# Kernel optimization log

Hardware: AMD Instinct MI355X
Metric: run time of the kernel (lower is better)

The kernel has to match this reference:

```python
import jax, jax.numpy as jnp
import numpy as np

# ---- constants mirroring the module config ----
TIMESTEPS = 1000
N_GT = 3            # GT phases {stable, pre-shock, shock}
NUM_EXPERTS = 6     # 2 sub-experts per GT phase; phase L -> experts {L, L+3}
LAMBDA_REG = 0.01
LAMBDA_LB = 0.01
PHASE_WEIGHTS = np.array([1.0, 5.0, 5.0], dtype=np.float32)


def _sinusoidal_embed(t, dim):
    # standard DDPM sinusoidal timestep embedding -> [B, dim]
    half = dim // 2
    freqs = jnp.exp(-jnp.log(10000.0) * jnp.arange(half, dtype=jnp.float32) / half)
    args = t.astype(jnp.float32)[:, None] * freqs[None, :]
    return jnp.concatenate([jnp.sin(args), jnp.cos(args)], axis=-1)


def _alphas_bar():
    betas = jnp.linspace(1e-4, 0.02, TIMESTEPS, dtype=jnp.float32)
    return jnp.cumprod(1.0 - betas)


def setup_inputs() -> dict:
    B, Tp, Tf, Df, Ds, dm, E, H = 512, 256, 64, 64, 32, 512, NUM_EXPERTS, 512
    key = jax.random.key(0)
    ks = jax.random.split(key, 16)
    s = 0.02  # init scale
    d_in = Df + 2 * dm  # noisy features + global ctx + t embedding
    return {
        'observed_data': jax.random.normal(ks[0], (B, Tp, Df), jnp.float32),
        'future_data':   jax.random.normal(ks[1], (B, Tf, Df), jnp.float32),
        'static_context': jax.random.normal(ks[2], (B, Ds), jnp.float32),
        'eps':           jax.random.normal(ks[3], (B, Tf, Df), jnp.float32),
        'phase_label':   jax.random.randint(ks[4], (B,), 0, N_GT),
        't':             jax.random.randint(ks[5], (B,), 0, TIMESTEPS),
        'W_enc':    jax.random.normal(ks[6], (Df, dm), jnp.float32) * s,
        'b_enc':    jnp.zeros((dm,), jnp.float32),
        'W_stat':   jax.random.normal(ks[7], (Ds, dm), jnp.float32) * s,
        'W_router': jax.random.normal(ks[8], (dm, E), jnp.float32) * s,
        'b_router': jnp.zeros((E,), jnp.float32),
        'W1': jax.random.normal(ks[9],  (E, d_in, H), jnp.float32) * s,
        'b1': jnp.zeros((E, H), jnp.float32),
        'W2': jax.random.normal(ks[10], (E, H, Df), jnp.float32) * s,
        'b2': jnp.zeros((E, Df), jnp.float32),
    }


def reference(observed_data, future_data, static_context, eps,
              W_enc, b_enc, W_stat, W_router, b_router,
              W1, b1, W2, b2, phase_label, t):
    B, Tf, Df = future_data.shape
    E = W1.shape[0]
    dm = W_enc.shape[1]

    # ---- frozen encoder (torch.no_grad in the original) ----
    ctx_seq = jax.nn.gelu(observed_data @ W_enc + (static_context @ W_stat)[:, None, :] + b_enc)  # [B,Tp,dm]
    global_ctx = ctx_seq.mean(axis=1)                                                             # [B,dm]
    ctx_seq = jax.lax.stop_gradient(ctx_seq)
    global_ctx = jax.lax.stop_gradient(global_ctx)

    # ---- router (trainable) ----
    router_logits = global_ctx @ W_router + b_router        # [B,E]
    router_probs = jax.nn.softmax(router_logits, axis=-1)

    # ---- GT-masked top-1 routing: phase p -> argmax over experts {p, p+3} ----
    selected = jnp.zeros((B,), jnp.int32)
    for p in range(N_GT):
        sub = jnp.stack([router_probs[:, p], router_probs[:, p + N_GT]], axis=1)  # [B,2]
        winner = p + N_GT * jnp.argmax(sub, axis=1).astype(jnp.int32)
        selected = jnp.where(phase_label == p, winner, selected)

    # ---- diffusion scheduler: add_noise ----
    ab = _alphas_bar()[t]                                   # [B]
    noisy_fut = (jnp.sqrt(ab)[:, None, None] * future_data
                 + jnp.sqrt(1.0 - ab)[:, None, None] * eps)  # [B,Tf,Df]

    # ---- expert backbones: run all E experts densely, then gather routed output ----
    t_emb = _sinusoidal_embed(t, dm)                        # [B,dm]
    cond = jnp.concatenate([
        noisy_fut,
        jnp.broadcast_to(global_ctx[:, None, :], (B, Tf, dm)),
        jnp.broadcast_to(t_emb[:, None, :],      (B, Tf, dm)),
    ], axis=-1)                                             # [B,Tf,Din]
    h = jax.nn.gelu(jnp.einsum('btd,edh->ebth', cond, W1) + b1[:, None, None, :])
    outputs_all = jnp.einsum('ebth,ehf->ebtf', h, W2) + b2[:, None, None, :]  # [E,B,Tf,Df]

    pred = outputs_all[selected, jnp.arange(B)]             # [B,Tf,Df] gradient-surgery dispatch
    loss_raw = jnp.mean((pred - eps) ** 2, axis=(1, 2))     # per-sample MSE, [B]

    # weighted_loss * count/B summed over experts == mean(loss_raw * w[selected%3])
    lw = jnp.asarray(PHASE_WEIGHTS)
    w_sample = lw[selected % N_GT]
    total_loss = jnp.mean(loss_raw * w_sample)

    # ---- consistency regularization on a fixed 4-sample subset ----
    S = min(B, 4)
    out_sub = outputs_all[:, :S]                            # [E,S,Tf,Df]
    chain = jnp.float32(0.0)
    for i in [0, 1, 3, 4]:
        if i + 1 < E:
            chain += jnp.mean((out_sub[i] - out_sub[i + 1]) ** 2)
    for i in range(N_GT):
        if i + N_GT < E:
            chain += jnp.mean((out_sub[i] - out_sub[i + N_GT]) ** 2)
    diff = out_sub[:, :, 1:] - out_sub[:, :, :-1]
    smooth = jnp.sum(jnp.mean(diff ** 2, axis=(1, 2, 3)))
    total_loss += (chain + 0.5 * smooth) * LAMBDA_REG

    # ---- load-balance loss ----
    onehot = (selected[:, None] == jnp.arange(E)[None, :]).astype(jnp.float32)  # [B,E]
    f = onehot.mean(axis=0)
    P = router_probs.mean(axis=0)
    total_loss += LAMBDA_LB * E * jnp.sum(f * P)

    return total_loss
```

## Files before the change

### kernel.cpp

```cpp
#include <hip/hip_runtime.h>

typedef float  f32x4 __attribute__((ext_vector_type(4)));
typedef short  s16x8 __attribute__((ext_vector_type(8)));
typedef unsigned short u16;
typedef u16    u16x4 __attribute__((ext_vector_type(4)));

#define TIMESTEPS 1000

#define WS_ALPHAS   0
#define WS_FREQS    1024
#define WS_PROBS    1536
#define WS_SELECTED 4608
#define WS_LOSSB    5632
#define WS_PARTS    7680
#define WS_FLAG     7700
#define WS_XC       270336
#define WS_HSTAT    532480
#define WS_HSTAT2   794624
#define WS_OUTSUB   806912
#define WS_U16BYTE  3620864
#define WS_BIAS     2691072
#define U_WENCT     0
#define U_W1T       32768
#define U_W2T       3375104

__device__ __forceinline__ u16 f2bf(float x){
    unsigned u = __builtin_bit_cast(unsigned, x);
    unsigned r = (u + 0x7FFFu + ((u >> 16) & 1u)) >> 16;
    return (u16)r;
}

__device__ __forceinline__ float gelu_f(float x){
    float x2 = x * x;
    float t  = x * fmaf(0.035677408136f, x2, 0.7978845608028654f);
    float ex = __builtin_amdgcn_exp2f(t * 2.885390081777927f);
    float r  = __builtin_amdgcn_rcpf(ex + 1.0f);
    return fmaf(-x, r, x);
}

__device__ __forceinline__ void mfma16(f32x4& c, s16x8 a, s16x8 b){
    asm volatile("v_mfma_f32_16x16x32_bf16 %0, %1, %2, %0" : "+v"(c) : "v"(a), "v"(b));
}

__global__ __launch_bounds__(256) void k0T(const float* __restrict__ Wenc,
                                           const float* __restrict__ W1,
                                           const float* __restrict__ W2,
                                           const float* __restrict__ stat,
                                           const float* __restrict__ Wstat,
                                           const float* __restrict__ benc,
                                           u16* __restrict__ uws,
                                           float* __restrict__ ws){
    __shared__ float sT[32][33];
    int bid = blockIdx.x, tid = threadIdx.x;
    const int t1 = 6*34*16, t2 = t1 + 6*16*2, t3 = t2 + 2*16;
    if(bid == t3){
        __shared__ float sp[256];
        for(int k = tid; k < 256; k += 256)
            ws[WS_FREQS + k] = expf(-logf(10000.0f) * (float)k / 256.0f);
        float p = 1.f;
        #pragma unroll
        for(int r = 0; r < 4; r++){
            int i = tid*4 + r;
            if(i < TIMESTEPS){
                float beta = 0.0001f + (0.02f - 0.0001f) * ((float)i / 999.0f);
                p *= (1.0f - beta);
            }
        }
        sp[tid] = p;
        __syncthreads();
        for(int st = 1; st < 256; st <<= 1){
            float v = (tid >= st) ? sp[tid - st] : 1.0f;
            __syncthreads();
            sp[tid] *= v;
            __syncthreads();
        }
        float run = (tid == 0) ? 1.0f : sp[tid - 1];
        for(int r = 0; r < 4; r++){
            int i = tid*4 + r;
            if(i < TIMESTEPS){
                float beta = 0.0001f + (0.02f - 0.0001f) * ((float)i / 999.0f);
                run *= (1.0f - beta);
                ws[WS_ALPHAS + i] = run;
            }
        }
        return;
    }
    if(bid > t3){
        __shared__ float sSt[8*32];
        int g = bid - t3 - 1;
        int b0 = g*8;
        sSt[tid & 255] = stat[b0*32 + (tid & 255)];
        __syncthreads();
        #pragma unroll
        for(int half = 0; half < 2; half++){
            int j = tid + half*256;
            float acc[8] = {0,0,0,0,0,0,0,0};
            for(int s = 0; s < 32; s++){
                float wv = Wstat[s*512 + j];
                #pragma unroll
                for(int bb = 0; bb < 8; bb++) acc[bb] += sSt[bb*32 + s] * wv;
            }
            float bz = benc[j];
            #pragma unroll
            for(int bb = 0; bb < 8; bb++)
                ws[WS_BIAS + (b0 + bb)*512 + j] = acc[bb] + bz;
        }
        return;
    }
    const float* src; u16* dst; int K, J, kt, jt;
    if(bid < t1){
        int e = bid / 544, r = bid % 544; kt = r / 16; jt = r % 16;
        src = W1 + (size_t)e*1088*512; dst = uws + U_W1T + (size_t)e*512*1088; K = 1088; J = 512;
    } else if(bid < t2){
        int r = bid - t1; int e = r / 32; r %= 32; kt = r / 2; jt = r % 2;
        src = W2 + (size_t)e*512*64; dst = uws + U_W2T + (size_t)e*64*512; K = 512; J = 64;
    } else {
        int r = bid - t2; kt = r / 16; jt = r % 16;
        src = Wenc; dst = uws + U_WENCT; K = 64; J = 512;
    }
    int ty = tid >> 5, tx = tid & 31;
    #pragma unroll
    for(int i = 0; i < 4; i++)
        sT[ty + i*8][tx] = src[(size_t)(kt*32 + ty + i*8)*J + jt*32 + tx];
    __syncthreads();
    #pragma unroll
    for(int i = 0; i < 4; i++)
        dst[(size_t)(jt*32 + ty + i*8)*K + kt*32 + tx] = f2bf(sT[tx][ty + i*8]);
}

#define PADX 72
__global__ __launch_bounds__(512) void k1_enc(const float* __restrict__ obs,
        const u16* __restrict__ uws, const float* __restrict__ Wr,
        const float* __restrict__ br, const int* __restrict__ phase,
        const int* __restrict__ t_arr, float* __restrict__ ws){
    __shared__ u16  sX[256 * PADX];
    __shared__ float sBias[512];
    __shared__ float sG[512];
    __shared__ float sRed[8][6];
    int b = blockIdx.x, tid = threadIdx.x;
    {
        int row = tid >> 1, c0 = (tid & 1) * 32;
        const f32x4* src = (const f32x4*)&obs[((size_t)b*256 + row)*64 + c0];
        u16* dst = &sX[row*PADX + c0];
        #pragma unroll
        for(int i = 0; i < 8; i++){
            f32x4 v = src[i];
            u16x4 pk; pk.x = f2bf(v.x); pk.y = f2bf(v.y); pk.z = f2bf(v.z); pk.w = f2bf(v.w);
            *(u16x4*)(dst + i*4) = pk;
        }
    }
    sBias[tid] = ws[WS_BIAS + b*512 + tid];
    __syncthreads();
    int w = tid >> 6, l = tid & 63, lr = l & 15, lk = (l >> 4) * 8;
    const u16* wencT = uws + U_WENCT;
    s16x8 bf[4][2];
    float bias[4];
    #pragma unroll
    for(int n = 0; n < 4; n++){
        int col = w*64 + n*16 + lr;
        bf[n][0] = *(const s16x8*)&wencT[col*64 + lk];
        bf[n][1] = *(const s16x8*)&wencT[col*64 + 32 + lk];
        bias[n]  = sBias[col];
    }
    float cac[4] = {0.f, 0.f, 0.f, 0.f};
    for(int mt = 0; mt < 16; mt++){
        s16x8 a0 = *(const s16x8*)&sX[(mt*16 + lr)*PADX + lk];
        s16x8 a1 = *(const s16x8*)&sX[(mt*16 + lr)*PADX + 32 + lk];
        #pragma unroll
        for(int n = 0; n < 4; n++){
            f32x4 acc = {bias[n], bias[n], bias[n], bias[n]};
            mfma16(acc, a0, bf[n][0]);
            mfma16(acc, a1, bf[n][1]);
            cac[n] += gelu_f(acc.x) + gelu_f(acc.y) + gelu_f(acc.z) + gelu_f(acc.w);
        }
    }
    #pragma unroll
    for(int n = 0; n < 4; n++){
        cac[n] += __shfl_xor(cac[n], 16);
        cac[n] += __shfl_xor(cac[n], 32);
    }
    if(l < 16){
        #pragma unroll
        for(int n = 0; n < 4; n++)
            sG[w*64 + n*16 + l] = cac[n] * (1.0f/256.0f);
    }
    __syncthreads();
    float gv = sG[tid];
    u16* XC = (u16*)(ws + WS_XC);
    XC[b*1024 + tid] = f2bf(gv);
    int tv = t_arr[b];
    {
        float fr = ws[WS_FREQS + (tid & 255)];
        float ang = (float)tv * fr;
        XC[b*1024 + 512 + tid] = f2bf((tid < 256) ? sinf(ang) : cosf(ang));
    }
    float p6[6];
    #pragma unroll
    for(int e = 0; e < 6; e++) p6[e] = gv * Wr[tid*6 + e];
    #pragma unroll
    for(int off = 32; off > 0; off >>= 1)
        #pragma unroll
        for(int e = 0; e < 6; e++) p6[e] += __shfl_down(p6[e], off);
    if(l == 0)
        #pragma unroll
        for(int e = 0; e < 6; e++) sRed[w][e] = p6[e];
    __syncthreads();
    if(tid == 0){
        float logit[6], mx = -1e30f;
        #pragma unroll
        for(int e = 0; e < 6; e++){
            float s = 0.f;
            #pragma unroll
            for(int q = 0; q < 8; q++) s += sRed[q][e];
            logit[e] = s + br[e];
            mx = fmaxf(mx, logit[e]);
        }
        float s = 0.f, p[6];
        #pragma unroll
        for(int e = 0; e < 6; e++){ p[e] = expf(logit[e] - mx); s += p[e]; }
        float inv = 1.0f / s;
        #pragma unroll
        for(int e = 0; e < 6; e++) ws[WS_PROBS + b*6 + e] = p[e] * inv;
        int ph = phase[b];
        int sel = ph + ((logit[ph + 3] > logit[ph]) ? 3 : 0);
        ((int*)ws)[WS_SELECTED + b] = sel;
    }
}

__global__ __launch_bounds__(256) void k3_hstat(const u16* __restrict__ uws,
        const float* __restrict__ b1, float* __restrict__ ws){
    __shared__ int sSrc[64], sDst[64];
    __shared__ int sCnt[8][6], sBase[8][6], sSec[6], sTot[6];
    __shared__ int sChunk[16][3];
    __shared__ int sNch;
    int bid = blockIdx.x, tid = threadIdx.x;
    int w = tid >> 6, l = tid & 63;
    int* wsi = (int*)ws;
    if(bid == 0 && tid == 0) wsi[WS_FLAG] = 0;
    int sv0 = wsi[WS_SELECTED + tid];
    int sv1 = wsi[WS_SELECTED + 256 + tid];
    unsigned long long mym0 = 0, mym1 = 0;
    #pragma unroll
    for(int e = 0; e < 6; e++){
        unsigned long long m0 = __ballot(sv0 == e);
        unsigned long long m1 = __ballot(sv1 == e);
        if(l == 0){ sCnt[w][e] = __popcll(m0); sCnt[4 + w][e] = __popcll(m1); }
        if(sv0 == e) mym0 = m0;
        if(sv1 == e) mym1 = m1;
    }
    if(tid < 64){ sSrc[tid] = 0; sDst[tid] = -1; }
    __syncthreads();
    if(tid == 0){
        int o = 0;
        for(int e = 0; e < 6; e++){
            sSec[e] = o; int t0 = 0;
            for(int g = 0; g < 8; g++){ sBase[g][e] = o; o += sCnt[g][e]; t0 += sCnt[g][e]; }
            sTot[e] = t0; o += 4;
        }
        int nch = 0;
        for(int e = 0; e < 6; e++){
            int len = sTot[e] + 4, st = sSec[e];
            for(int s = 0; s < len; s += 64){
                sChunk[nch][0] = e; sChunk[nch][1] = st + s;
                sChunk[nch][2] = (len - s < 64) ? (len - s) : 64; nch++;
            }
        }
        sNch = nch;
    }
    __syncthreads();
    int c = bid >> 3, jt = bid & 7;
    if(c >= sNch) return;
    int e     = sChunk[c][0];
    int start = sChunk[c][1];
    int len   = sChunk[c][2];
    {
        int rank = __popcll(mym0 & ((1ull << l) - 1ull));
        int pos = sBase[w][sv0] + rank - start;
        if(pos >= 0 && pos < len){ sSrc[pos] = tid; sDst[pos] = WS_HSTAT + tid*512; }
    }
    {
        int rank = __popcll(mym1 & ((1ull << l) - 1ull));
        int pos = sBase[4 + w][sv1] + rank - start;
        if(pos >= 0 && pos < len){ sSrc[pos] = 256 + tid; sDst[pos] = WS_HSTAT + (256 + tid)*512; }
    }
    if(tid < 24){
        int ea = tid >> 2, ba = tid & 3;
        int pos = sSec[ea] + sTot[ea] + ba - start;
        if(pos >= 0 && pos < len){ sSrc[pos] = ba; sDst[pos] = WS_HSTAT2 + (ea*4 + ba)*512; }
    }
    __syncthreads();
    int lr = l & 15, lk = (l >> 4) * 8;
    int col = jt*64 + w*16 + lr;
    const u16* XC = (const u16*)(ws + WS_XC);
    const u16* rowA[4];
    #pragma unroll
    for(int mt = 0; mt < 4; mt++)
        rowA[mt] = XC + (size_t)sSrc[mt*16 + lr]*1024 + lk;
    const u16* bp = uws + U_W1T + ((size_t)e*512 + col)*1088 + 64 + lk;
    f32x4 acc[4];
    {
        float bv = b1[e*512 + col];
        f32x4 z = {bv, bv, bv, bv};
        #pragma unroll
        for(int mt = 0; mt < 4; mt++) acc[mt] = z;
    }
    #pragma unroll 4
    for(int ks = 0; ks < 32; ks++){
        s16x8 bb = *(const s16x8*)(bp + ks*32);
        s16x8 a0 = *(const s16x8*)(rowA[0] + ks*32);
        s16x8 a1 = *(const s16x8*)(rowA[1] + ks*32);
        s16x8 a2 = *(const s16x8*)(rowA[2] + ks*32);
        s16x8 a3 = *(const s16x8*)(rowA[3] + ks*32);
        mfma16(acc[0], a0, bb);
        mfma16(acc[1], a1, bb);
        mfma16(acc[2], a2, bb);
        mfma16(acc[3], a3, bb);
    }
    #pragma unroll
    for(int mt = 0; mt < 4; mt++){
        #pragma unroll
        for(int rg = 0; rg < 4; rg++){
            int r = mt*16 + (l >> 4)*4 + rg;
            int d = sDst[r];
            if(d >= 0) ws[d + col] = acc[mt][rg];
        }
    }
}

#define PADN 72
#define PADH 520
__global__ __launch_bounds__(512) void k4_ffn(const float* __restrict__ fut,
        const float* __restrict__ eps, const int* __restrict__ t_arr,
        const u16* __restrict__ uws, const float* __restrict__ b2,
        float* __restrict__ ws){
    __shared__ u16 sN[64 * PADN];
    __shared__ u16 sH[64 * PADH];
    __shared__ float sHs[512];
    __shared__ float sRed[8];
    int tid = threadIdx.x, bid = blockIdx.x;
    int* wsi = (int*)ws;
    int b, e, store;
    if(bid < 24){ e = bid >> 2; b = bid & 3; store = 1; }
    else { b = bid - 24; e = wsi[WS_SELECTED + b]; store = 0; }
    sHs[tid] = store ? ws[WS_HSTAT2 + (e*4 + b)*512 + tid] : ws[WS_HSTAT + b*512 + tid];
    int tv = t_arr[b];
    float ab = ws[WS_ALPHAS + tv];
    float sa = sqrtf(ab), sb = sqrtf(1.0f - ab);
    {
        int r = tid >> 3, c0 = (tid & 7) * 8;
        const f32x4* pf = (const f32x4*)&fut[((size_t)b*64 + r)*64 + c0];
        const f32x4* pe = (const f32x4*)&eps[((size_t)b*64 + r)*64 + c0];
        f32x4 f0 = pf[0], f1 = pf[1], e0 = pe[0], e1 = pe[1];
        u16x4 p0, p1;
        p0.x = f2bf(sa*f0.x + sb*e0.x); p0.y = f2bf(sa*f0.y + sb*e0.y);
        p0.z = f2bf(sa*f0.z + sb*e0.z); p0.w = f2bf(sa*f0.w + sb*e0.w);
        p1.x = f2bf(sa*f1.x + sb*e1.x); p1.y = f2bf(sa*f1.y + sb*e1.y);
        p1.z = f2bf(sa*f1.z + sb*e1.z); p1.w = f2bf(sa*f1.w + sb*e1.w);
        *(u16x4*)&sN[r*PADN + c0]     = p0;
        *(u16x4*)&sN[r*PADN + c0 + 4] = p1;
    }
    __syncthreads();
    int w = tid >> 6, l = tid & 63, lr = l & 15, lk = (l >> 4) * 8;
    const u16* w1T = uws + U_W1T;
    const u16* w2T = uws + U_W2T;
    s16x8 aw[4][2];
    #pragma unroll
    for(int mt = 0; mt < 4; mt++){
        int jrow = w*64 + mt*16 + lr;
        aw[mt][0] = *(const s16x8*)&w1T[((size_t)e*512 + jrow)*1088 + lk];
        aw[mt][1] = *(const s16x8*)&w1T[((size_t)e*512 + jrow)*1088 + 32 + lk];
    }
    #pragma unroll
    for(int nt = 0; nt < 4; nt++){
        s16x8 nb0 = *(const s16x8*)&sN[(nt*16 + lr)*PADN + lk];
        s16x8 nb1 = *(const s16x8*)&sN[(nt*16 + lr)*PADN + 32 + lk];
        #pragma unroll
        for(int mt = 0; mt < 4; mt++){
            int j0 = w*64 + mt*16 + (l >> 4)*4;
            f32x4 acc = *(const f32x4*)&sHs[j0];
            mfma16(acc, aw[mt][0], nb0);
            mfma16(acc, aw[mt][1], nb1);
            u16x4 pk;
            pk.x = f2bf(gelu_f(acc.x)); pk.y = f2bf(gelu_f(acc.y));
            pk.z = f2bf(gelu_f(acc.z)); pk.w = f2bf(gelu_f(acc.w));
            *(u16x4*)&sH[(nt*16 + lr)*PADH + j0] = pk;
        }
    }
    __syncthreads();
    int mtg = (w >> 2) << 1;
    int nt  = w & 3;
    f32x4 oacc[2];
    {
        float bz = b2[e*64 + nt*16 + lr];
        f32x4 z = {bz, bz, bz, bz}; oacc[0] = z; oacc[1] = z;
    }
    for(int ks = 0; ks < 16; ks++){
        s16x8 bb = *(const s16x8*)&w2T[((size_t)e*64 + nt*16 + lr)*512 + ks*32 + lk];
        #pragma unroll
        for(int i = 0; i < 2; i++){
            s16x8 a = *(const s16x8*)&sH[((mtg + i)*16 + lr)*PADH + ks*32 + lk];
            mfma16(oacc[i], a, bb);
        }
    }
    if(store){
        #pragma unroll
        for(int i = 0; i < 2; i++)
            #pragma unroll
            for(int rg = 0; rg < 4; rg++){
                int row = (mtg + i)*16 + (l >> 4)*4 + rg;
                int col = nt*16 + lr;
                ws[WS_OUTSUB + (e*4 + b)*4096 + row*64 + col] = oacc[i][rg];
            }
    } else {
        float ls = 0.f;
        #pragma unroll
        for(int i = 0; i < 2; i++)
            #pragma unroll
            for(int rg = 0; rg < 4; rg++){
                int row = (mtg + i)*16 + (l >> 4)*4 + rg;
                int col = nt*16 + lr;
                float d = oacc[i][rg] - eps[((size_t)b*64 + row)*64 + col];
                ls += d*d;
            }
        #pragma unroll
        for(int off = 32; off > 0; off >>= 1) ls += __shfl_down(ls, off);
        if(l == 0) sRed[w] = ls;
        __syncthreads();
        if(tid == 0){
            float s = 0.f;
            #pragma unroll
            for(int q = 0; q < 8; q++) s += sRed[q];
            const float pw[3] = {1.f, 5.f, 5.f};
            ws[WS_LOSSB + b] = (s * (1.0f/4096.0f)) * pw[e % 3];
        }
    }
}

__global__ __launch_bounds__(256) void k5_final(float* __restrict__ ws, float* __restrict__ out){
    int bid = blockIdx.x, tid = threadIdx.x;
    int* wsi = (int*)ws;
    if(bid < 13){
        __shared__ float red[256];
        float s = 0.f;
        if(bid < 7){
            const int pa[7] = {0,1,3,4,0,1,2};
            const int pb[7] = {1,2,4,5,3,4,5};
            const float* A  = &ws[WS_OUTSUB + pa[bid]*16384];
            const float* Bp = &ws[WS_OUTSUB + pb[bid]*16384];
            for(int i = tid; i < 4096; i += 256){
                f32x4 a = *(const f32x4*)&A[i*4];
                f32x4 c = *(const f32x4*)&Bp[i*4];
                f32x4 d = a - c;
                s += d.x*d.x + d.y*d.y + d.z*d.z + d.w*d.w;
            }
            s *= (1.0f/16384.0f);
        } else {
            int e = bid - 7;
            const float* O = &ws[WS_OUTSUB + e*16384];
            for(int i = tid; i < 4*63*16; i += 256){
                int sm = i / (63*16); int r = i % (63*16);
                int tf = r / 16; int f4 = (r % 16) * 4;
                f32x4 a = *(const f32x4*)&O[(sm*64 + tf + 1)*64 + f4];
                f32x4 c = *(const f32x4*)&O[(sm*64 + tf)*64 + f4];
                f32x4 d = a - c;
                s += d.x*d.x + d.y*d.y + d.z*d.z + d.w*d.w;
            }
            s *= (1.0f/16128.0f) * 0.5f;
        }
        red[tid] = s;
        __syncthreads();
        for(int st = 128; st > 0; st >>= 1){
            if(tid < st) red[tid] += red[tid + st];
            __syncthreads();
        }
        if(tid == 0){
            ws[WS_PARTS + bid] = red[0];
            __threadfence();
            atomicAdd(&wsi[WS_FLAG], 1);
        }
        return;
    }
    if(tid == 0){
        while(atomicAdd(&wsi[WS_FLAG], 0) < 13) __builtin_amdgcn_s_sleep(2);
    }
    __syncthreads();
    __threadfence();
    __shared__ float sW[4];
    __shared__ float sF[4][6], sP[4][6];
    int w = tid >> 6, l = tid & 63;
    int sel0 = wsi[WS_SELECTED + tid];
    int sel1 = wsi[WS_SELECTED + 256 + tid];
    float lv = ws[WS_LOSSB + tid] + ws[WS_LOSSB + 256 + tid];
    float pv[6], cf[6];
    #pragma unroll
    for(int e = 0; e < 6; e++){
        pv[e] = ws[WS_PROBS + tid*6 + e] + ws[WS_PROBS + (256 + tid)*6 + e];
        cf[e] = ((sel0 == e) ? 1.f : 0.f) + ((sel1 == e) ? 1.f : 0.f);
    }
    #pragma unroll
    for(int off = 32; off > 0; off >>= 1){
        lv += __shfl_down(lv, off);
        #pragma unroll
        for(int e = 0; e < 6; e++){
            pv[e] += __shfl_down(pv[e], off);
            cf[e] += __shfl_down(cf[e], off);
        }
    }
    if(l == 0){
        sW[w] = lv;
        #pragma unroll
        for(int e = 0; e < 6; e++){ sF[w][e] = cf[e]; sP[w][e] = pv[e]; }
    }
    __syncthreads();
    if(tid == 0){
        float total = 0.f;
        for(int q = 0; q < 4; q++) total += sW[q];
        total *= (1.0f/512.0f);
        volatile float* vp = ws + WS_PARTS;
        float reg = 0.f;
        for(int p = 0; p < 13; p++) reg += vp[p];
        total += 0.01f * reg;
        float lb = 0.f;
        for(int e = 0; e < 6; e++){
            float f = 0.f, pp = 0.f;
            for(int q = 0; q < 4; q++){ f += sF[q][e]; pp += sP[q][e]; }
            lb += (f * (1.0f/512.f)) * (pp * (1.0f/512.f));
        }
        out[0] = total + 0.01f * 6.0f * lb;
    }
}

extern "C" void kernel_launch(void* const* d_in, const int* in_sizes, int n_in,
                              void* d_out, int out_size, void* d_ws, size_t ws_size,
                              hipStream_t stream){
    const float* obs  = (const float*)d_in[0];
    const float* fut  = (const float*)d_in[1];
    const float* stat = (const float*)d_in[2];
    const float* eps  = (const float*)d_in[3];
    const int*   phase= (const int*)d_in[4];
    const int*   t    = (const int*)d_in[5];
    const float* Wenc = (const float*)d_in[6];
    const float* benc = (const float*)d_in[7];
    const float* Wstat= (const float*)d_in[8];
    const float* Wr   = (const float*)d_in[9];
    const float* br   = (const float*)d_in[10];
    const float* W1   = (const float*)d_in[11];
    const float* b1   = (const float*)d_in[12];
    const float* W2   = (const float*)d_in[13];
    const float* b2   = (const float*)d_in[14];
    float* ws  = (float*)d_ws;
    u16*   uws = (u16*)((char*)d_ws + WS_U16BYTE);
    float* out = (float*)d_out;

    k0T<<<3553, 256, 0, stream>>>(Wenc, W1, W2, stat, Wstat, benc, uws, ws);
    k1_enc<<<512, 512, 0, stream>>>(obs, uws, Wr, br, phase, t, ws);
    k3_hstat<<<112, 256, 0, stream>>>(uws, b1, ws);
    k4_ffn<<<536, 512, 0, stream>>>(fut, eps, t, uws, b2, ws);
    k5_final<<<14, 256, 0, stream>>>(ws, out);
}
```

Measured before the change: 104.1 us.

## Fuse W1/W2 weight transposes into the encoder kernel via interleaved blocks

The preprocessing kernel is split in two. A small first kernel now computes the frequency table, the alpha schedule, the Wenc transpose and the static-context bias. The large W1/W2 bf16 transpose work moves into the encoder kernel, whose 1024-thread blocks alternate between encoder work (even block ids) and four transpose tiles each (odd and trailing ids). The aim is to overlap the memory-bound weight transpose with the MFMA-heavy encoder and to shorten the serial chain of large launches. The trade-off is that the encoder block grows to 1024 threads with each wave handling half the columns, and the shared-memory union may reduce occupancy.

```diff
diff --git a/kernel.cpp b/kernel.cpp
--- a/kernel.cpp
+++ b/kernel.cpp
@@ -18,8 +18,8 @@
 #define WS_HSTAT    532480
 #define WS_HSTAT2   794624
 #define WS_OUTSUB   806912
+#define WS_BIAS     2691072
 #define WS_U16BYTE  3620864
-#define WS_BIAS     2691072
 #define U_WENCT     0
 #define U_W1T       32768
 #define U_W2T       3375104
@@ -42,18 +42,14 @@
     asm volatile("v_mfma_f32_16x16x32_bf16 %0, %1, %2, %0" : "+v"(c) : "v"(a), "v"(b));
 }
 
-__global__ __launch_bounds__(256) void k0T(const float* __restrict__ Wenc,
-                                           const float* __restrict__ W1,
-                                           const float* __restrict__ W2,
+__global__ __launch_bounds__(256) void k0a(const float* __restrict__ Wenc,
                                            const float* __restrict__ stat,
                                            const float* __restrict__ Wstat,
                                            const float* __restrict__ benc,
                                            u16* __restrict__ uws,
                                            float* __restrict__ ws){
-    __shared__ float sT[32][33];
     int bid = blockIdx.x, tid = threadIdx.x;
-    const int t1 = 6*34*16, t2 = t1 + 6*16*2, t3 = t2 + 2*16;
-    if(bid == t3){
+    if(bid == 0){
         __shared__ float sp[256];
         for(int k = tid; k < 256; k += 256)
             ws[WS_FREQS + k] = expf(-logf(10000.0f) * (float)k / 256.0f);
@@ -85,89 +81,107 @@
         }
         return;
     }
-    if(bid > t3){
-        __shared__ float sSt[8*32];
-        int g = bid - t3 - 1;
-        int b0 = g*8;
-        sSt[tid & 255] = stat[b0*32 + (tid & 255)];
+    if(bid <= 32){
+        __shared__ float sT[32][33];
+        int r = bid - 1, kt = r >> 4, jt = r & 15;
+        int ty = tid >> 5, tx = tid & 31;
+        #pragma unroll
+        for(int i = 0; i < 4; i++)
+            sT[ty + i*8][tx] = Wenc[(size_t)(kt*32 + ty + i*8)*512 + jt*32 + tx];
         __syncthreads();
         #pragma unroll
-        for(int half = 0; half < 2; half++){
-            int j = tid + half*256;
-            float acc[8] = {0,0,0,0,0,0,0,0};
-            for(int s = 0; s < 32; s++){
-                float wv = Wstat[s*512 + j];
-                #pragma unroll
-                for(int bb = 0; bb < 8; bb++) acc[bb] += sSt[bb*32 + s] * wv;
-            }
-            float bz = benc[j];
-            #pragma unroll
-            for(int bb = 0; bb < 8; bb++)
-                ws[WS_BIAS + (b0 + bb)*512 + j] = acc[bb] + bz;
-        }
+        for(int i = 0; i < 4; i++)
+            uws[U_WENCT + (size_t)(jt*32 + ty + i*8)*64 + kt*32 + tx] = f2bf(sT[tx][ty + i*8]);
         return;
     }
-    const float* src; u16* dst; int K, J, kt, jt;
-    if(bid < t1){
-        int e = bid / 544, r = bid % 544; kt = r / 16; jt = r % 16;
-        src = W1 + (size_t)e*1088*512; dst = uws + U_W1T + (size_t)e*512*1088; K = 1088; J = 512;
-    } else if(bid < t2){
-        int r = bid - t1; int e = r / 32; r %= 32; kt = r / 2; jt = r % 2;
-        src = W2 + (size_t)e*512*64; dst = uws + U_W2T + (size_t)e*64*512; K = 512; J = 64;
-    } else {
-        int r = bid - t2; kt = r / 16; jt = r % 16;
-        src = Wenc; dst = uws + U_WENCT; K = 64; J = 512;
-    }
-    int ty = tid >> 5, tx = tid & 31;
-    #pragma unroll
-    for(int i = 0; i < 4; i++)
-        sT[ty + i*8][tx] = src[(size_t)(kt*32 + ty + i*8)*J + jt*32 + tx];
-    __syncthreads();
-    #pragma unroll
-    for(int i = 0; i < 4; i++)
-        dst[(size_t)(jt*32 + ty + i*8)*K + kt*32 + tx] = f2bf(sT[tx][ty + i*8]);
+    __shared__ float sSt[8*32];
+    int g = bid - 33;
+    int b0 = g*8;
+    sSt[tid] = stat[b0*32 + tid];
+    __syncthreads();
+    #pragma unroll
+    for(int half = 0; half < 2; half++){
+        int j = tid + half*256;
+        float acc[8] = {0,0,0,0,0,0,0,0};
+        for(int s = 0; s < 32; s++){
+            float wv = Wstat[s*512 + j];
+            #pragma unroll
+            for(int bb = 0; bb < 8; bb++) acc[bb] += sSt[bb*32 + s] * wv;
+        }
+        float bz = benc[j];
+        #pragma unroll
+        for(int bb = 0; bb < 8; bb++)
+            ws[WS_BIAS + (b0 + bb)*512 + j] = acc[bb] + bz;
+    }
 }
 
 #define PADX 72
-__global__ __launch_bounds__(512) void k1_enc(const float* __restrict__ obs,
-        const u16* __restrict__ uws, const float* __restrict__ Wr,
-        const float* __restrict__ br, const int* __restrict__ phase,
-        const int* __restrict__ t_arr, float* __restrict__ ws){
-    __shared__ u16  sX[256 * PADX];
-    __shared__ float sBias[512];
-    __shared__ float sG[512];
-    __shared__ float sRed[8][6];
-    int b = blockIdx.x, tid = threadIdx.x;
+__global__ __launch_bounds__(1024) void kMain(const float* __restrict__ obs,
+        const float* __restrict__ W1, const float* __restrict__ W2,
+        const u16* __restrict__ uws_c, u16* __restrict__ uws,
+        const float* __restrict__ Wr, const float* __restrict__ br,
+        const int* __restrict__ phase, const int* __restrict__ t_arr,
+        float* __restrict__ ws){
+    __shared__ union {
+        struct { u16 sX[256*PADX]; float sBias[512]; float sG[512]; float sRed[16][6]; } k1;
+        float sT[4][32][33];
+    } sm;
+    int bid = blockIdx.x, tid = threadIdx.x;
+
+    if(!(bid < 1024 && (bid & 1) == 0)){
+        int tix4 = (bid < 1024) ? (bid >> 1) : (512 + bid - 1024);
+        int t = tix4*4 + (tid >> 8);
+        int sub = tid >> 8;
+        int ty = (tid >> 5) & 7, tx = tid & 31;
+        const float* src; u16* dst; int K, J, kt, jt;
+        if(t < 3264){
+            int e = t / 544, r = t % 544; kt = r >> 4; jt = r & 15;
+            src = W1 + (size_t)e*1088*512; dst = uws + U_W1T + (size_t)e*512*1088; K = 1088; J = 512;
+        } else {
+            int t2 = t - 3264; int e = t2 >> 5; int r = t2 & 31; kt = r >> 1; jt = r & 1;
+            src = W2 + (size_t)e*512*64; dst = uws + U_W2T + (size_t)e*64*512; K = 512; J = 64;
+        }
+        #pragma unroll
+        for(int i = 0; i < 4; i++)
+            sm.sT[sub][ty + i*8][tx] = src[(size_t)(kt*32 + ty + i*8)*J + jt*32 + tx];
+        __syncthreads();
+        #pragma unroll
+        for(int i = 0; i < 4; i++)
+            dst[(size_t)(jt*32 + ty + i*8)*K + kt*32 + tx] = f2bf(sm.sT[sub][tx][ty + i*8]);
+        return;
+    }
+
+    int b = bid >> 1;
     {
-        int row = tid >> 1, c0 = (tid & 1) * 32;
+        int row = tid >> 2, c0 = (tid & 3) * 16;
         const f32x4* src = (const f32x4*)&obs[((size_t)b*256 + row)*64 + c0];
-        u16* dst = &sX[row*PADX + c0];
-        #pragma unroll
-        for(int i = 0; i < 8; i++){
+        u16* dst = &sm.k1.sX[row*PADX + c0];
+        #pragma unroll
+        for(int i = 0; i < 4; i++){
             f32x4 v = src[i];
             u16x4 pk; pk.x = f2bf(v.x); pk.y = f2bf(v.y); pk.z = f2bf(v.z); pk.w = f2bf(v.w);
             *(u16x4*)(dst + i*4) = pk;
         }
     }
-    sBias[tid] = ws[WS_BIAS + b*512 + tid];
+    if(tid < 512) sm.k1.sBias[tid] = ws[WS_BIAS + b*512 + tid];
     __syncthreads();
     int w = tid >> 6, l = tid & 63, lr = l & 15, lk = (l >> 4) * 8;
-    const u16* wencT = uws + U_WENCT;
-    s16x8 bf[4][2];
-    float bias[4];
-    #pragma unroll
-    for(int n = 0; n < 4; n++){
-        int col = w*64 + n*16 + lr;
+    const u16* wencT = uws_c + U_WENCT;
+    s16x8 bf[2][2];
+    float bias[2];
+    #pragma unroll
+    for(int n = 0; n < 2; n++){
+        int col = w*32 + n*16 + lr;
         bf[n][0] = *(const s16x8*)&wencT[col*64 + lk];
         bf[n][1] = *(const s16x8*)&wencT[col*64 + 32 + lk];
-        bias[n]  = sBias[col];
-    }
-    float cac[4] = {0.f, 0.f, 0.f, 0.f};
+        bias[n]  = sm.k1.sBias[col];
+    }
+    float cac[2] = {0.f, 0.f};
     for(int mt = 0; mt < 16; mt++){
-        s16x8 a0 = *(const s16x8*)&sX[(mt*16 + lr)*PADX + lk];
-        s16x8 a1 = *(const s16x8*)&sX[(mt*16 + lr)*PADX + 32 + lk];
-        #pragma unroll
-        for(int n = 0; n < 4; n++){
+        s16x8 a0 = *(const s16x8*)&sm.k1.sX[(mt*16 + lr)*PADX + lk];
+        s16x8 a1 = *(const s16x8*)&sm.k1.sX[(mt*16 + lr)*PADX + 32 + lk];
+        #pragma unroll
+        for(int n = 0; n < 2; n++){
             f32x4 acc = {bias[n], bias[n], bias[n], bias[n]};
             mfma16(acc, a0, bf[n][0]);
             mfma16(acc, a1, bf[n][1]);
@@ -175,35 +189,35 @@
         }
     }
     #pragma unroll
-    for(int n = 0; n < 4; n++){
+    for(int n = 0; n < 2; n++){
         cac[n] += __shfl_xor(cac[n], 16);
         cac[n] += __shfl_xor(cac[n], 32);
     }
     if(l < 16){
         #pragma unroll
-        for(int n = 0; n < 4; n++)
-            sG[w*64 + n*16 + l] = cac[n] * (1.0f/256.0f);
-    }
-    __syncthreads();
-    float gv = sG[tid];
-    u16* XC = (u16*)(ws + WS_XC);
-    XC[b*1024 + tid] = f2bf(gv);
-    int tv = t_arr[b];
-    {
+        for(int n = 0; n < 2; n++)
+            sm.k1.sG[w*32 + n*16 + l] = cac[n] * (1.0f/256.0f);
+    }
+    __syncthreads();
+    float p6[6] = {0,0,0,0,0,0};
+    if(tid < 512){
+        float gv = sm.k1.sG[tid];
+        u16* XC = (u16*)(ws + WS_XC);
+        XC[b*1024 + tid] = f2bf(gv);
+        int tv = t_arr[b];
         float fr = ws[WS_FREQS + (tid & 255)];
         float ang = (float)tv * fr;
         XC[b*1024 + 512 + tid] = f2bf((tid < 256) ? sinf(ang) : cosf(ang));
-    }
-    float p6[6];
-    #pragma unroll
-    for(int e = 0; e < 6; e++) p6[e] = gv * Wr[tid*6 + e];
-    #pragma unroll
-    for(int off = 32; off > 0; off >>= 1)
-        #pragma unroll
-        for(int e = 0; e < 6; e++) p6[e] += __shfl_down(p6[e], off);
-    if(l == 0)
-        #pragma unroll
-        for(int e = 0; e < 6; e++) sRed[w][e] = p6[e];
+        #pragma unroll
+        for(int e = 0; e < 6; e++) p6[e] = gv * Wr[tid*6 + e];
+        #pragma unroll
+        for(int off = 32; off > 0; off >>= 1)
+            #pragma unroll
+            for(int e = 0; e < 6; e++) p6[e] += __shfl_down(p6[e], off);
+        if(l == 0)
+            #pragma unroll
+            for(int e = 0; e < 6; e++) sm.k1.sRed[w][e] = p6[e];
+    }
     __syncthreads();
     if(tid == 0){
         float logit[6], mx = -1e30f;
@@ -211,7 +225,7 @@
         for(int e = 0; e < 6; e++){
             float s = 0.f;
             #pragma unroll
-            for(int q = 0; q < 8; q++) s += sRed[q][e];
+            for(int q = 0; q < 8; q++) s += sm.k1.sRed[q][e];
             logit[e] = s + br[e];
             mx = fmaxf(mx, logit[e]);
         }
@@ -552,8 +566,8 @@
     u16*   uws = (u16*)((char*)d_ws + WS_U16BYTE);
     float* out = (float*)d_out;
 
-    k0T<<<3553, 256, 0, stream>>>(Wenc, W1, W2, stat, Wstat, benc, uws, ws);
-    k1_enc<<<512, 512, 0, stream>>>(obs, uws, Wr, br, phase, t, ws);
+    k0a<<<97, 256, 0, stream>>>(Wenc, stat, Wstat, benc, uws, ws);
+    kMain<<<1376, 1024, 0, stream>>>(obs, W1, W2, uws, uws, Wr, br, phase, t, ws);
     k3_hstat<<<112, 256, 0, stream>>>(uws, b1, ws);
     k4_ffn<<<536, 512, 0, stream>>>(fut, eps, t, uws, b2, ws);
     k5_final<<<14, 256, 0, stream>>>(ws, out);
```

Result: slower. 122.5 us (+17.7%).

## Enlarge transpose tiles and split encoder and FFN blocks in half

Applied to the files above, without the earlier changes.

The weight-transpose kernel now uses 64x64 tiles with vectorized loads and stores, which cuts the block count from 3553 to 937. The encoder kernel splits each sample's 256 timesteps across two blocks. It combines the two partial GELU sums through a workspace buffer and an atomic counter, so the last-arriving block finishes the router work. The FFN kernel splits each sample's 64 future steps across two blocks and accumulates the per-sample loss with atomicAdd, applying the phase weight in the final kernel. The aim is more parallelism and fewer, wider memory transactions, at the cost of extra atomics, fences and workspace traffic.

```diff
diff --git a/kernel.cpp b/kernel.cpp
--- a/kernel.cpp
+++ b/kernel.cpp
@@ -12,14 +12,16 @@
 #define WS_PROBS    1536
 #define WS_SELECTED 4608
 #define WS_LOSSB    5632
+#define WS_FLAG1    6144
 #define WS_PARTS    7680
 #define WS_FLAG     7700
+#define WS_P0       8192
 #define WS_XC       270336
 #define WS_HSTAT    532480
 #define WS_HSTAT2   794624
 #define WS_OUTSUB   806912
+#define WS_BIAS     2691072
 #define WS_U16BYTE  3620864
-#define WS_BIAS     2691072
 #define U_WENCT     0
 #define U_W1T       32768
 #define U_W2T       3375104
@@ -42,21 +44,18 @@
     asm volatile("v_mfma_f32_16x16x32_bf16 %0, %1, %2, %0" : "+v"(c) : "v"(a), "v"(b));
 }
 
-__global__ __launch_bounds__(256) void k0T(const float* __restrict__ Wenc,
-                                           const float* __restrict__ W1,
-                                           const float* __restrict__ W2,
-                                           const float* __restrict__ stat,
-                                           const float* __restrict__ Wstat,
-                                           const float* __restrict__ benc,
-                                           u16* __restrict__ uws,
-                                           float* __restrict__ ws){
-    __shared__ float sT[32][33];
+__global__ __launch_bounds__(256) void k0(const float* __restrict__ Wenc,
+        const float* __restrict__ W1, const float* __restrict__ W2,
+        const float* __restrict__ stat, const float* __restrict__ Wstat,
+        const float* __restrict__ benc, u16* __restrict__ uws, float* __restrict__ ws){
+    __shared__ float sT[64][65];
+    float* sp = &sT[0][0];
     int bid = blockIdx.x, tid = threadIdx.x;
-    const int t1 = 6*34*16, t2 = t1 + 6*16*2, t3 = t2 + 2*16;
-    if(bid == t3){
-        __shared__ float sp[256];
-        for(int k = tid; k < 256; k += 256)
-            ws[WS_FREQS + k] = expf(-logf(10000.0f) * (float)k / 256.0f);
+    int* wsi = (int*)ws;
+    if(bid == 0){
+        wsi[WS_FLAG1 + tid] = 0; wsi[WS_FLAG1 + 256 + tid] = 0;
+        ws[WS_LOSSB + tid] = 0.f; ws[WS_LOSSB + 256 + tid] = 0.f;
+        ws[WS_FREQS + tid] = expf(-logf(10000.0f) * (float)tid / 256.0f);
         float p = 1.f;
         #pragma unroll
         for(int r = 0; r < 4; r++){
@@ -85,11 +84,27 @@
         }
         return;
     }
-    if(bid > t3){
-        __shared__ float sSt[8*32];
-        int g = bid - t3 - 1;
-        int b0 = g*8;
-        sSt[tid & 255] = stat[b0*32 + (tid & 255)];
+    if(bid <= 8){
+        int jt = bid - 1;
+        int r = tid >> 2, c0 = (tid & 3) * 16;
+        #pragma unroll
+        for(int i = 0; i < 4; i++)
+            *(f32x4*)&sT[r][c0 + i*4] = *(const f32x4*)&Wenc[(size_t)r*512 + jt*64 + c0 + i*4];
+        __syncthreads();
+        u16* dst = uws + U_WENCT + (size_t)(jt*64 + r)*64;
+        #pragma unroll
+        for(int i = 0; i < 4; i++){
+            u16x4 pk;
+            pk.x = f2bf(sT[c0 + i*4 + 0][r]); pk.y = f2bf(sT[c0 + i*4 + 1][r]);
+            pk.z = f2bf(sT[c0 + i*4 + 2][r]); pk.w = f2bf(sT[c0 + i*4 + 3][r]);
+            *(u16x4*)&dst[c0 + i*4] = pk;
+        }
+        return;
+    }
+    if(bid <= 72){
+        float* sSt = sp;
+        int g = bid - 9, b0 = g*8;
+        sSt[tid] = stat[b0*32 + tid];
         __syncthreads();
         #pragma unroll
         for(int half = 0; half < 2; half++){
@@ -107,25 +122,28 @@
         }
         return;
     }
+    int t = bid - 73;
     const float* src; u16* dst; int K, J, kt, jt;
-    if(bid < t1){
-        int e = bid / 544, r = bid % 544; kt = r / 16; jt = r % 16;
+    if(t < 816){
+        int e = t / 136, r = t % 136; kt = r >> 3; jt = r & 7;
         src = W1 + (size_t)e*1088*512; dst = uws + U_W1T + (size_t)e*512*1088; K = 1088; J = 512;
-    } else if(bid < t2){
-        int r = bid - t1; int e = r / 32; r %= 32; kt = r / 2; jt = r % 2;
+    } else {
+        int t2 = t - 816; int e = t2 >> 3; kt = t2 & 7; jt = 0;
         src = W2 + (size_t)e*512*64; dst = uws + U_W2T + (size_t)e*64*512; K = 512; J = 64;
-    } else {
-        int r = bid - t2; kt = r / 16; jt = r % 16;
-        src = Wenc; dst = uws + U_WENCT; K = 64; J = 512;
-    }
-    int ty = tid >> 5, tx = tid & 31;
+    }
+    int r = tid >> 2, c0 = (tid & 3) * 16;
     #pragma unroll
     for(int i = 0; i < 4; i++)
-        sT[ty + i*8][tx] = src[(size_t)(kt*32 + ty + i*8)*J + jt*32 + tx];
-    __syncthreads();
-    #pragma unroll
-    for(int i = 0; i < 4; i++)
-        dst[(size_t)(jt*32 + ty + i*8)*K + kt*32 + tx] = f2bf(sT[tx][ty + i*8]);
+        *(f32x4*)&sT[r][c0 + i*4] = *(const f32x4*)&src[(size_t)(kt*64 + r)*J + jt*64 + c0 + i*4];
+    __syncthreads();
+    u16* d2 = dst + (size_t)(jt*64 + r)*K + kt*64;
+    #pragma unroll
+    for(int i = 0; i < 4; i++){
+        u16x4 pk;
+        pk.x = f2bf(sT[c0 + i*4 + 0][r]); pk.y = f2bf(sT[c0 + i*4 + 1][r]);
+        pk.z = f2bf(sT[c0 + i*4 + 2][r]); pk.w = f2bf(sT[c0 + i*4 + 3][r]);
+        *(u16x4*)&d2[c0 + i*4] = pk;
+    }
 }
 
 #define PADX 72
@@ -133,17 +151,19 @@
         const u16* __restrict__ uws, const float* __restrict__ Wr,
         const float* __restrict__ br, const int* __restrict__ phase,
         const int* __restrict__ t_arr, float* __restrict__ ws){
-    __shared__ u16  sX[256 * PADX];
+    __shared__ u16  sX[128 * PADX];
     __shared__ float sBias[512];
     __shared__ float sG[512];
     __shared__ float sRed[8][6];
-    int b = blockIdx.x, tid = threadIdx.x;
+    __shared__ int sOld;
+    int bid = blockIdx.x, b = bid >> 1, q = bid & 1, tid = threadIdx.x;
+    int* wsi = (int*)ws;
     {
-        int row = tid >> 1, c0 = (tid & 1) * 32;
-        const f32x4* src = (const f32x4*)&obs[((size_t)b*256 + row)*64 + c0];
+        int row = tid >> 2, c0 = (tid & 3) * 16;
+        const f32x4* src = (const f32x4*)&obs[((size_t)(b*256 + q*128 + row))*64 + c0];
         u16* dst = &sX[row*PADX + c0];
         #pragma unroll
-        for(int i = 0; i < 8; i++){
+        for(int i = 0; i < 4; i++){
             f32x4 v = src[i];
             u16x4 pk; pk.x = f2bf(v.x); pk.y = f2bf(v.y); pk.z = f2bf(v.z); pk.w = f2bf(v.w);
             *(u16x4*)(dst + i*4) = pk;
@@ -163,7 +183,7 @@
         bias[n]  = sBias[col];
     }
     float cac[4] = {0.f, 0.f, 0.f, 0.f};
-    for(int mt = 0; mt < 16; mt++){
+    for(int mt = 0; mt < 8; mt++){
         s16x8 a0 = *(const s16x8*)&sX[(mt*16 + lr)*PADX + lk];
         s16x8 a1 = *(const s16x8*)&sX[(mt*16 + lr)*PADX + 32 + lk];
         #pragma unroll
@@ -182,10 +202,18 @@
     if(l < 16){
         #pragma unroll
         for(int n = 0; n < 4; n++)
-            sG[w*64 + n*16 + l] = cac[n] * (1.0f/256.0f);
-    }
-    __syncthreads();
-    float gv = sG[tid];
+            sG[w*64 + n*16 + l] = cac[n];
+    }
+    __syncthreads();
+    ws[(q ? WS_HSTAT : WS_P0) + b*512 + tid] = sG[tid];
+    __threadfence();
+    __syncthreads();
+    if(tid == 0) sOld = atomicAdd(&wsi[WS_FLAG1 + b], 1);
+    __syncthreads();
+    if(sOld == 0) return;
+    __threadfence();
+    const float* op = &ws[(q ? WS_P0 : WS_HSTAT) + b*512];
+    float gv = (sG[tid] + op[tid]) * (1.0f/256.0f);
     u16* XC = (u16*)(ws + WS_XC);
     XC[b*1024 + tid] = f2bf(gv);
     int tv = t_arr[b];
@@ -211,7 +239,7 @@
         for(int e = 0; e < 6; e++){
             float s = 0.f;
             #pragma unroll
-            for(int q = 0; q < 8; q++) s += sRed[q][e];
+            for(int qq = 0; qq < 8; qq++) s += sRed[qq][e];
             logit[e] = s + br[e];
             mx = fmaxf(mx, logit[e]);
         }
@@ -223,7 +251,7 @@
         for(int e = 0; e < 6; e++) ws[WS_PROBS + b*6 + e] = p[e] * inv;
         int ph = phase[b];
         int sel = ph + ((logit[ph + 3] > logit[ph]) ? 3 : 0);
-        ((int*)ws)[WS_SELECTED + b] = sel;
+        wsi[WS_SELECTED + b] = sel;
     }
 }
 
@@ -333,23 +361,24 @@
         const float* __restrict__ eps, const int* __restrict__ t_arr,
         const u16* __restrict__ uws, const float* __restrict__ b2,
         float* __restrict__ ws){
-    __shared__ u16 sN[64 * PADN];
-    __shared__ u16 sH[64 * PADH];
+    __shared__ u16 sN[32 * PADN];
+    __shared__ u16 sH[32 * PADH];
     __shared__ float sHs[512];
     __shared__ float sRed[8];
     int tid = threadIdx.x, bid = blockIdx.x;
     int* wsi = (int*)ws;
-    int b, e, store;
-    if(bid < 24){ e = bid >> 2; b = bid & 3; store = 1; }
-    else { b = bid - 24; e = wsi[WS_SELECTED + b]; store = 0; }
+    int b, e, store, half;
+    if(bid < 48){ int idx = bid >> 1; half = bid & 1; e = idx >> 2; b = idx & 3; store = 1; }
+    else { int r = bid - 48; b = r >> 1; half = r & 1; e = wsi[WS_SELECTED + b]; store = 0; }
+    int tf0 = half * 32;
     sHs[tid] = store ? ws[WS_HSTAT2 + (e*4 + b)*512 + tid] : ws[WS_HSTAT + b*512 + tid];
     int tv = t_arr[b];
     float ab = ws[WS_ALPHAS + tv];
     float sa = sqrtf(ab), sb = sqrtf(1.0f - ab);
-    {
+    if(tid < 256){
         int r = tid >> 3, c0 = (tid & 7) * 8;
-        const f32x4* pf = (const f32x4*)&fut[((size_t)b*64 + r)*64 + c0];
-        const f32x4* pe = (const f32x4*)&eps[((size_t)b*64 + r)*64 + c0];
+        const f32x4* pf = (const f32x4*)&fut[((size_t)b*64 + tf0 + r)*64 + c0];
+        const f32x4* pe = (const f32x4*)&eps[((size_t)b*64 + tf0 + r)*64 + c0];
         f32x4 f0 = pf[0], f1 = pf[1], e0 = pe[0], e1 = pe[1];
         u16x4 p0, p1;
         p0.x = f2bf(sa*f0.x + sb*e0.x); p0.y = f2bf(sa*f0.y + sb*e0.y);
@@ -371,7 +400,7 @@
         aw[mt][1] = *(const s16x8*)&w1T[((size_t)e*512 + jrow)*1088 + 32 + lk];
     }
     #pragma unroll
-    for(int nt = 0; nt < 4; nt++){
+    for(int nt = 0; nt < 2; nt++){
         s16x8 nb0 = *(const s16x8*)&sN[(nt*16 + lr)*PADN + lk];
         s16x8 nb1 = *(const s16x8*)&sN[(nt*16 + lr)*PADN + 32 + lk];
         #pragma unroll
@@ -387,41 +416,34 @@
         }
     }
     __syncthreads();
-    int mtg = (w >> 2) << 1;
-    int nt  = w & 3;
-    f32x4 oacc[2];
+    int mt_o = w >> 2;
+    int nt_o = w & 3;
+    f32x4 oacc;
     {
-        float bz = b2[e*64 + nt*16 + lr];
-        f32x4 z = {bz, bz, bz, bz}; oacc[0] = z; oacc[1] = z;
+        float bz = b2[e*64 + nt_o*16 + lr];
+        f32x4 z = {bz, bz, bz, bz}; oacc = z;
     }
     for(int ks = 0; ks < 16; ks++){
-        s16x8 bb = *(const s16x8*)&w2T[((size_t)e*64 + nt*16 + lr)*512 + ks*32 + lk];
-        #pragma unroll
-        for(int i = 0; i < 2; i++){
-            s16x8 a = *(const s16x8*)&sH[((mtg + i)*16 + lr)*PADH + ks*32 + lk];
-            mfma16(oacc[i], a, bb);
-        }
+        s16x8 bb = *(const s16x8*)&w2T[((size_t)e*64 + nt_o*16 + lr)*512 + ks*32 + lk];
+        s16x8 a  = *(const s16x8*)&sH[(mt_o*16 + lr)*PADH + ks*32 + lk];
+        mfma16(oacc, a, bb);
     }
     if(store){
         #pragma unroll
-        for(int i = 0; i < 2; i++)
-            #pragma unroll
-            for(int rg = 0; rg < 4; rg++){
-                int row = (mtg + i)*16 + (l >> 4)*4 + rg;
-                int col = nt*16 + lr;
-                ws[WS_OUTSUB + (e*4 + b)*4096 + row*64 + col] = oacc[i][rg];
-            }
+        for(int rg = 0; rg < 4; rg++){
+            int row = tf0 + mt_o*16 + (l >> 4)*4 + rg;
+            int col = nt_o*16 + lr;
+            ws[WS_OUTSUB + (e*4 + b)*4096 + row*64 + col] = oacc[rg];
+        }
     } else {
         float ls = 0.f;
         #pragma unroll
-        for(int i = 0; i < 2; i++)
-            #pragma unroll
-            for(int rg = 0; rg < 4; rg++){
-                int row = (mtg + i)*16 + (l >> 4)*4 + rg;
-                int col = nt*16 + lr;
-                float d = oacc[i][rg] - eps[((size_t)b*64 + row)*64 + col];
-                ls += d*d;
-            }
+        for(int rg = 0; rg < 4; rg++){
+            int row = tf0 + mt_o*16 + (l >> 4)*4 + rg;
+            int col = nt_o*16 + lr;
+            float d = oacc[rg] - eps[((size_t)b*64 + row)*64 + col];
+            ls += d*d;
+        }
         #pragma unroll
         for(int off = 32; off > 0; off >>= 1) ls += __shfl_down(ls, off);
         if(l == 0) sRed[w] = ls;
@@ -429,9 +451,8 @@
         if(tid == 0){
             float s = 0.f;
             #pragma unroll
-            for(int q = 0; q < 8; q++) s += sRed[q];
-            const float pw[3] = {1.f, 5.f, 5.f};
-            ws[WS_LOSSB + b] = (s * (1.0f/4096.0f)) * pw[e % 3];
+            for(int qq = 0; qq < 8; qq++) s += sRed[qq];
+            atomicAdd(&ws[WS_LOSSB + b], s);
         }
     }
 }
@@ -490,7 +511,10 @@
     int w = tid >> 6, l = tid & 63;
     int sel0 = wsi[WS_SELECTED + tid];
     int sel1 = wsi[WS_SELECTED + 256 + tid];
-    float lv = ws[WS_LOSSB + tid] + ws[WS_LOSSB + 256 + tid];
+    float wg0 = (sel0 == 0 || sel0 == 3) ? 1.f : 5.f;
+    float wg1 = (sel1 == 0 || sel1 == 3) ? 1.f : 5.f;
+    float lv = ws[WS_LOSSB + tid] * (1.0f/4096.0f) * wg0
+             + ws[WS_LOSSB + 256 + tid] * (1.0f/4096.0f) * wg1;
     float pv[6], cf[6];
     #pragma unroll
     for(int e = 0; e < 6; e++){
@@ -552,9 +576,9 @@
     u16*   uws = (u16*)((char*)d_ws + WS_U16BYTE);
     float* out = (float*)d_out;
 
-    k0T<<<3553, 256, 0, stream>>>(Wenc, W1, W2, stat, Wstat, benc, uws, ws);
-    k1_enc<<<512, 512, 0, stream>>>(obs, uws, Wr, br, phase, t, ws);
+    k0<<<937, 256, 0, stream>>>(Wenc, W1, W2, stat, Wstat, benc, uws, ws);
+    k1_enc<<<1024, 512, 0, stream>>>(obs, uws, Wr, br, phase, t, ws);
     k3_hstat<<<112, 256, 0, stream>>>(uws, b1, ws);
-    k4_ffn<<<536, 512, 0, stream>>>(fut, eps, t, uws, b2, ws);
+    k4_ffn<<<1072, 512, 0, stream>>>(fut, eps, t, uws, b2, ws);
     k5_final<<<14, 256, 0, stream>>>(ws, out);
 }
```

After: 343.5 us. 230% more time.
